# Optimization experiments

Measured on AMD Instinct MI355X. Metric: run time of the kernel, lower is better.

## Reference

```python
import jax, jax.numpy as jnp
import numpy as np

N = 50000
E = 400000
IN_DIM = 256
H1, D1 = 4, 128   # gat1: heads=4, hidden=128, concat -> 512
H2, D2 = 1, 64    # gat2: heads=1, out=64, concat=False
NEG_SLOPE = 0.2


def setup_inputs() -> dict:
    key = jax.random.key(0)
    ks = jax.random.split(key, 12)
    x = jax.random.normal(ks[0], (N, IN_DIM), dtype=jnp.float32)
    edge_index = jax.random.randint(ks[1], (2, E), 0, N, dtype=jnp.int64)
    edge_attr = jax.random.normal(ks[2], (E,), dtype=jnp.float32)
    # Glorot-ish init for weights, zeros for biases (as in PyG GATConv)
    def glorot(k, shape):
        fan = shape[0] + shape[-1]
        return jax.random.normal(k, shape, dtype=jnp.float32) * jnp.sqrt(2.0 / fan)
    W1 = glorot(ks[3], (IN_DIM, H1 * D1))
    a1_src = glorot(ks[4], (H1, D1))
    a1_dst = glorot(ks[5], (H1, D1))
    b1 = jnp.zeros((H1 * D1,), dtype=jnp.float32)
    W2 = glorot(ks[6], (H1 * D1, H2 * D2))
    a2_src = glorot(ks[7], (H2, D2))
    a2_dst = glorot(ks[8], (H2, D2))
    b2 = jnp.zeros((D2,), dtype=jnp.float32)
    return {"x": x, "edge_index": edge_index, "edge_attr": edge_attr,
            "W1": W1, "a1_src": a1_src, "a1_dst": a1_dst, "b1": b1,
            "W2": W2, "a2_src": a2_src, "a2_dst": a2_dst, "b2": b2}


def _gat_layer(x, src, dst, W, a_s, a_d, b, heads, d, concat):
    n = x.shape[0]
    h = (x @ W).reshape(n, heads, d)                      # [N,H,D]
    alpha_s = jnp.einsum('nhd,hd->nh', h, a_s)            # [N,H]
    alpha_d = jnp.einsum('nhd,hd->nh', h, a_d)
    e = jax.nn.leaky_relu(alpha_s[src] + alpha_d[dst], NEG_SLOPE)  # [Etot,H]
    # segment softmax over incoming edges of each dst node
    emax = jax.ops.segment_max(e, dst, num_segments=n)
    ex = jnp.exp(e - emax[dst])
    denom = jax.ops.segment_sum(ex, dst, num_segments=n)
    alpha = ex / (denom[dst] + 1e-16)                     # [Etot,H]
    msg = h[src] * alpha[:, :, None]                      # [Etot,H,D]
    out = jax.ops.segment_sum(msg, dst, num_segments=n)   # [N,H,D]
    out = out.reshape(n, heads * d) if concat else out.mean(axis=1)
    return out + b


def reference(x, edge_index, edge_attr, W1, a1_src, a1_dst, b1,
              W2, a2_src, a2_dst, b2):
    # edge_attr is ignored (GATConv built without edge_dim)
    loop = jnp.arange(N, dtype=edge_index.dtype)          # PyG add_self_loops=True
    src = jnp.concatenate([edge_index[0], loop])
    dst = jnp.concatenate([edge_index[1], loop])
    h = _gat_layer(x, src, dst, W1, a1_src, a1_dst, b1, H1, D1, True)
    h = jax.nn.elu(h)
    out = _gat_layer(h, src, dst, W2, a2_src, a2_dst, b2, H2, D2, False)
    return out
```

## Files before the change

### kernel.cpp

```cpp
#include <hip/hip_runtime.h>
#include <cstdint>

typedef unsigned short u16;
typedef short bf16x8_t __attribute__((ext_vector_type(8)));
typedef float f32x4_t __attribute__((ext_vector_type(4)));

#define DEVFN __device__ __forceinline__

DEVFN u16 f2bf(float f) {
  unsigned u = __builtin_bit_cast(unsigned, f);
  u = (u + 0x7fffu + ((u >> 16) & 1u)) >> 16;
  return (u16)u;
}
DEVFN float bf2f(u16 s) {
  unsigned u = ((unsigned)s) << 16;
  return __builtin_bit_cast(float, u);
}
DEVFN unsigned pk2bf(float a, float b) {
  return (unsigned)f2bf(a) | ((unsigned)f2bf(b) << 16);
}

DEVFN void gload_lds16(const u16* g, u16* l) {
  __builtin_amdgcn_global_load_lds(
      (const __attribute__((address_space(1))) void*)g,
      (__attribute__((address_space(3))) void*)l, 16, 0, 0);
}

__global__ void prep_kernel(const float* __restrict__ W1, const float* __restrict__ W2,
                            const int* __restrict__ edst,
                            u16* __restrict__ w1t, u16* __restrict__ w2t,
                            int* __restrict__ cnt, int e) {
  int b = blockIdx.x;
  if (b < 512) {
    int idx = b * 256 + threadIdx.x;
    int k = idx >> 9, m = idx & 511;
    w1t[m * 256 + k] = f2bf(W1[idx]);
  } else if (b < 512 + 128) {
    int idx = (b - 512) * 256 + threadIdx.x;
    int k = idx >> 6, m = idx & 63;
    w2t[m * 512 + k] = f2bf(W2[idx]);
  } else {
    int i = (b - 640) * 256 + threadIdx.x;
    if (i < e) atomicAdd(&cnt[edst[i]], 1);
  }
}

template<int BM, int BN, int WROWS, int K, int BK, int NP, int H, int DH>
__global__ __launch_bounds__(256) void gemm1_alpha_kernel(
    const float* __restrict__ A, const u16* __restrict__ BT, u16* __restrict__ C,
    const float* __restrict__ a_s, const float* __restrict__ a_d,
    float* __restrict__ as_out, float* __restrict__ ad_out, int M)
{
  constexpr int N = NP * BN;
  constexpr int WM = BM / WROWS;
  constexpr int MF = WM / 16;
  constexpr int NF = BN / 16;
  constexpr int KK = BK / 32;
  __shared__ __align__(16) u16 sA[BM][BK];
  __shared__ __align__(16) u16 sB[BN][BK];

  const int tid = threadIdx.x;
  const int lane = tid & 63;
  const int wr = tid >> 6;

  const int bid = blockIdx.x;
  const int xcd = bid & 7;
  const int rest = bid >> 3;
  const int p = rest & (NP - 1);
  const int rb = rest / NP;
  const int r = rb * 8 + xcd;
  const int NRB = (M + BM - 1) / BM;
  if (r >= NRB) return;
  const int brow = r * BM;
  const int bcol = p * BN;

  f32x4_t acc[MF][NF];
#pragma unroll
  for (int i = 0; i < MF; ++i)
#pragma unroll
    for (int j = 0; j < NF; ++j) acc[i][j] = f32x4_t{0.f, 0.f, 0.f, 0.f};

  const int rsel = lane & 15;
  const int kgrp = (lane >> 4) * 8;

#pragma unroll
  for (int k0 = 0; k0 < K; k0 += BK) {
    constexpr int RA = BM * BK / 2048;
#pragma unroll
    for (int c = 0; c < RA; ++c) {
      int q = c * 256 + tid;
      int row = q * 8 / BK;
      int col8 = (q * 8) % BK;
      int gr = brow + row; gr = gr < M ? gr : M - 1;
      const float* src = A + (size_t)gr * K + k0 + col8;
      float4 v0 = *reinterpret_cast<const float4*>(src);
      float4 v1 = *reinterpret_cast<const float4*>(src + 4);
      uint4 pk;
      pk.x = pk2bf(v0.x, v0.y);
      pk.y = pk2bf(v0.z, v0.w);
      pk.z = pk2bf(v1.x, v1.y);
      pk.w = pk2bf(v1.z, v1.w);
      *reinterpret_cast<uint4*>(&sA[row][col8]) = pk;
    }
    constexpr int RB = BN * BK / 2048;
#pragma unroll
    for (int c = 0; c < RB; ++c) {
      int t = c * 256 + tid;
      int row = t * 8 / BK;
      int col = (t * 8) % BK;
      gload_lds16(BT + (size_t)(bcol + row) * K + k0 + col, &sB[0][0] + t * 8);
    }
    __syncthreads();
#pragma unroll
    for (int kk = 0; kk < KK; ++kk) {
      bf16x8_t af[MF], bfr[NF];
#pragma unroll
      for (int i = 0; i < MF; ++i)
        af[i] = *reinterpret_cast<const bf16x8_t*>(&sA[wr * WM + i * 16 + rsel][kk * 32 + kgrp]);
#pragma unroll
      for (int j = 0; j < NF; ++j)
        bfr[j] = *reinterpret_cast<const bf16x8_t*>(&sB[j * 16 + rsel][kk * 32 + kgrp]);
#pragma unroll
      for (int i = 0; i < MF; ++i)
#pragma unroll
        for (int j = 0; j < NF; ++j)
          acc[i][j] = __builtin_amdgcn_mfma_f32_16x16x32_bf16(af[i], bfr[j], acc[i][j], 0, 0, 0);
    }
    __syncthreads();
  }

  const int crow0 = (lane >> 4) * 4;
  const int ccol = lane & 15;

#pragma unroll
  for (int i = 0; i < MF; ++i)
#pragma unroll
    for (int j = 0; j < NF; ++j)
#pragma unroll
      for (int rr = 0; rr < 4; ++rr) {
        int gr = brow + wr * WM + i * 16 + crow0 + rr;
        int gc = bcol + j * 16 + ccol;
        if (gr < M) C[(size_t)gr * N + gc] = f2bf(acc[i][j][rr]);
      }

  const int head = bcol / DH;
  float asv[NF], adv[NF];
#pragma unroll
  for (int j = 0; j < NF; ++j) {
    int gc = bcol + j * 16 + ccol;
    asv[j] = a_s[gc];
    adv[j] = a_d[gc];
  }
#pragma unroll
  for (int i = 0; i < MF; ++i) {
#pragma unroll
    for (int rr = 0; rr < 4; ++rr) {
      float ps = 0.f, pd = 0.f;
#pragma unroll
      for (int j = 0; j < NF; ++j) {
        float v = acc[i][j][rr];
        ps = fmaf(v, asv[j], ps);
        pd = fmaf(v, adv[j], pd);
      }
#pragma unroll
      for (int d = 1; d < 16; d <<= 1) {
        ps += __shfl_xor(ps, d, 64);
        pd += __shfl_xor(pd, d, 64);
      }
      if ((lane & 15) == 0) {
        int gr = brow + wr * WM + i * 16 + crow0 + rr;
        if (gr < M) {
          as_out[(size_t)gr * H + head] = ps;
          ad_out[(size_t)gr * H + head] = pd;
        }
      }
    }
  }
}

template<int BM, int BN, int WROWS, int K, int BK, int H, int DH>
__global__ __launch_bounds__(256) void gemm_alpha_kernel(
    const u16* __restrict__ A, const u16* __restrict__ BT, u16* __restrict__ C,
    const float* __restrict__ a_s, const float* __restrict__ a_d,
    float* __restrict__ as_out, float* __restrict__ ad_out, int M, int N)
{
  static_assert(BN == DH, "alpha store ownership");
  constexpr int WM = BM / WROWS;
  constexpr int MF = WM / 16;
  constexpr int NF = BN / 16;
  constexpr int KK = BK / 32;
  __shared__ __align__(16) u16 sA[BM][BK];
  __shared__ __align__(16) u16 sB[BN][BK];

  const int tid = threadIdx.x;
  const int lane = tid & 63;
  const int wr = tid >> 6;
  const int brow = blockIdx.x * BM;
  const int bcol = blockIdx.y * BN;

  f32x4_t acc[MF][NF];
#pragma unroll
  for (int i = 0; i < MF; ++i)
#pragma unroll
    for (int j = 0; j < NF; ++j) acc[i][j] = f32x4_t{0.f, 0.f, 0.f, 0.f};

  const int rsel = lane & 15;
  const int kgrp = (lane >> 4) * 8;

#pragma unroll
  for (int k0 = 0; k0 < K; k0 += BK) {
    constexpr int RA = BM * BK / 2048;
#pragma unroll
    for (int c = 0; c < RA; ++c) {
      int t = c * 256 + tid;
      int row = t * 8 / BK;
      int col = (t * 8) % BK;
      int gr = brow + row; gr = gr < M ? gr : M - 1;
      gload_lds16(A + (size_t)gr * K + k0 + col, &sA[0][0] + t * 8);
    }
    constexpr int RB = BN * BK / 2048;
#pragma unroll
    for (int c = 0; c < RB; ++c) {
      int t = c * 256 + tid;
      int row = t * 8 / BK;
      int col = (t * 8) % BK;
      gload_lds16(BT + (size_t)(bcol + row) * K + k0 + col, &sB[0][0] + t * 8);
    }
    __syncthreads();
#pragma unroll
    for (int kk = 0; kk < KK; ++kk) {
      bf16x8_t af[MF], bfr[NF];
#pragma unroll
      for (int i = 0; i < MF; ++i)
        af[i] = *reinterpret_cast<const bf16x8_t*>(&sA[wr * WM + i * 16 + rsel][kk * 32 + kgrp]);
#pragma unroll
      for (int j = 0; j < NF; ++j)
        bfr[j] = *reinterpret_cast<const bf16x8_t*>(&sB[j * 16 + rsel][kk * 32 + kgrp]);
#pragma unroll
      for (int i = 0; i < MF; ++i)
#pragma unroll
        for (int j = 0; j < NF; ++j)
          acc[i][j] = __builtin_amdgcn_mfma_f32_16x16x32_bf16(af[i], bfr[j], acc[i][j], 0, 0, 0);
    }
    __syncthreads();
  }

  const int crow0 = (lane >> 4) * 4;
  const int ccol = lane & 15;

#pragma unroll
  for (int i = 0; i < MF; ++i)
#pragma unroll
    for (int j = 0; j < NF; ++j)
#pragma unroll
      for (int rr = 0; rr < 4; ++rr) {
        int gr = brow + wr * WM + i * 16 + crow0 + rr;
        int gc = bcol + j * 16 + ccol;
        if (gr < M) C[(size_t)gr * N + gc] = f2bf(acc[i][j][rr]);
      }

  const int head = bcol / DH;
  float asv[NF], adv[NF];
#pragma unroll
  for (int j = 0; j < NF; ++j) {
    int gc = bcol + j * 16 + ccol;
    asv[j] = a_s[gc];
    adv[j] = a_d[gc];
  }
#pragma unroll
  for (int i = 0; i < MF; ++i) {
#pragma unroll
    for (int rr = 0; rr < 4; ++rr) {
      float ps = 0.f, pd = 0.f;
#pragma unroll
      for (int j = 0; j < NF; ++j) {
        float v = acc[i][j][rr];
        ps = fmaf(v, asv[j], ps);
        pd = fmaf(v, adv[j], pd);
      }
#pragma unroll
      for (int d = 1; d < 16; d <<= 1) {
        ps += __shfl_xor(ps, d, 64);
        pd += __shfl_xor(pd, d, 64);
      }
      if ((lane & 15) == 0) {
        int gr = brow + wr * WM + i * 16 + crow0 + rr;
        if (gr < M) {
          as_out[(size_t)gr * H + head] = ps;
          ad_out[(size_t)gr * H + head] = pd;
        }
      }
    }
  }
}

DEVFN int block_scan_256(int v, int tid, int* wsum) {
#pragma unroll
  for (int d = 1; d < 64; d <<= 1) {
    int u = __shfl_up(v, d, 64);
    if ((tid & 63) >= d) v += u;
  }
  if ((tid & 63) == 63) wsum[tid >> 6] = v;
  __syncthreads();
  int add = 0;
#pragma unroll
  for (int w = 0; w < 4; ++w) add += (w < (tid >> 6)) ? wsum[w] : 0;
  __syncthreads();
  return v + add;
}

__global__ __launch_bounds__(256) void scan_a_kernel(const int* __restrict__ cnt, int* __restrict__ bsum, int n) {
  __shared__ int ws4[4];
  int i = blockIdx.x * 256 + threadIdx.x;
  int v = (i < n) ? cnt[i] + 1 : 0;
  int incl = block_scan_256(v, threadIdx.x, ws4);
  if (threadIdx.x == 255) bsum[blockIdx.x] = incl;
}

__global__ __launch_bounds__(256) void scan_c_kernel(
    const int* __restrict__ cnt, const int* __restrict__ bsum,
    int* __restrict__ rowoff, int* __restrict__ cursor, int n)
{
  __shared__ int ws4[4];
  __shared__ int ws4b[4];
  __shared__ int base_sh;
  int pre = 0;
  for (int w = threadIdx.x; w < blockIdx.x; w += 256) pre += bsum[w];
#pragma unroll
  for (int d = 1; d < 64; d <<= 1) pre += __shfl_xor(pre, d, 64);
  if ((threadIdx.x & 63) == 0) ws4b[threadIdx.x >> 6] = pre;
  __syncthreads();
  if (threadIdx.x == 0) base_sh = ws4b[0] + ws4b[1] + ws4b[2] + ws4b[3];
  int i = blockIdx.x * 256 + threadIdx.x;
  int v = (i < n) ? cnt[i] + 1 : 0;
  int incl = block_scan_256(v, threadIdx.x, ws4);
  int off = base_sh + incl - v;
  if (i < n) {
    rowoff[i] = off;
    cursor[i] = off;
    if (i == n - 1) rowoff[n] = off + v;
  }
}

__global__ void scatter_kernel(const int* __restrict__ srcs, const int* __restrict__ dsts,
                               int* __restrict__ cursor, int* __restrict__ csr, int e, int n) {
  int i = blockIdx.x * 256 + threadIdx.x;
  if (i >= e + n) return;
  int s, d;
  if (i < e) { s = srcs[i]; d = dsts[i]; }
  else       { s = i - e; d = s; }
  int pos = atomicAdd(&cursor[d], 1);
  csr[pos] = s;
}

__global__ __launch_bounds__(256) void agg1_kernel(
    const u16* __restrict__ h1, const float* __restrict__ as1,
    const float* __restrict__ ad1, const int* __restrict__ rowoff,
    const int* __restrict__ csr, const float* __restrict__ b1,
    u16* __restrict__ out, int n)
{
  int node = (blockIdx.x * 256 + threadIdx.x) >> 6;
  int lane = threadIdx.x & 63;
  if (node >= n) return;
  const unsigned head = lane >> 4;
  const unsigned dimbase = lane * 8;
  int e0 = rowoff[node], e1 = rowoff[node + 1];
  float advn = ad1[((unsigned)node << 2) + head];

  float acc[8];
#pragma unroll
  for (int j = 0; j < 8; ++j) acc[j] = 0.f;
  float den = 0.f;

  for (int e = e0; e < e1; ++e) {
    unsigned s = (unsigned)csr[e];
    float t = as1[(s << 2) + head] + advn;
    float l = fmaxf(t, 0.2f * t);
    float ex = __expf(l);
    den += ex;
    bf16x8_t hv = *reinterpret_cast<const bf16x8_t*>(h1 + ((s << 9) + dimbase));
#pragma unroll
    for (int j = 0; j < 8; ++j) acc[j] = fmaf(ex, bf2f((u16)hv[j]), acc[j]);
  }

  float inv = 1.f / (den + 1e-16f);
  u16* orow = out + (((unsigned)node << 9) + dimbase);
#pragma unroll
  for (int j = 0; j < 8; ++j) {
    float v = acc[j] * inv + b1[dimbase + j];
    v = v > 0.f ? v : expm1f(v);
    orow[j] = f2bf(v);
  }
}

__global__ __launch_bounds__(256) void agg2_kernel(
    const u16* __restrict__ h2, const float* __restrict__ as2,
    const float* __restrict__ ad2, const int* __restrict__ rowoff,
    const int* __restrict__ csr, const float* __restrict__ b2,
    float* __restrict__ out, int n)
{
  int node = (blockIdx.x * 256 + threadIdx.x) >> 5;
  int l32 = threadIdx.x & 31;
  if (node >= n) return;
  int e0 = rowoff[node], e1 = rowoff[node + 1];
  float advn = ad2[node];

  float acc0 = 0.f, acc1 = 0.f, den = 0.f;
  for (int e = e0; e < e1; ++e) {
    unsigned s = (unsigned)csr[e];
    float t = as2[s] + advn;
    float l = fmaxf(t, 0.2f * t);
    float ex = __expf(l);
    den += ex;
    unsigned hv = *reinterpret_cast<const unsigned*>(h2 + (s << 6) + l32 * 2);
    acc0 = fmaf(ex, bf2f((u16)(hv & 0xffffu)), acc0);
    acc1 = fmaf(ex, bf2f((u16)(hv >> 16)), acc1);
  }
  float inv = 1.f / (den + 1e-16f);
  float2 o;
  o.x = acc0 * inv + b2[l32 * 2];
  o.y = acc1 * inv + b2[l32 * 2 + 1];
  *reinterpret_cast<float2*>(out + (((size_t)node) << 6) + l32 * 2) = o;
}

extern "C" void kernel_launch(void* const* d_in, const int* in_sizes, int n_in,
                              void* d_out, int out_size, void* d_ws, size_t ws_size,
                              hipStream_t stream) {
  const float* x   = (const float*)d_in[0];
  const int*   ei  = (const int*)d_in[1];
  const float* W1  = (const float*)d_in[3];
  const float* a1s = (const float*)d_in[4];
  const float* a1d = (const float*)d_in[5];
  const float* b1  = (const float*)d_in[6];
  const float* W2  = (const float*)d_in[7];
  const float* a2s = (const float*)d_in[8];
  const float* a2d = (const float*)d_in[9];
  const float* b2  = (const float*)d_in[10];
  float* out = (float*)d_out;

  const int IN_DIM = 256, H1D1 = 512, D2 = 64;
  const int N = in_sizes[0] / IN_DIM;
  const int E = in_sizes[1] / 2;

  char* ws = (char*)d_ws;
  size_t off = 0;
  auto alloc = [&](size_t bytes) -> void* {
    void* p = ws + off;
    off += (bytes + 255) & ~(size_t)255;
    return p;
  };
  u16*  w1t    = (u16*)alloc((size_t)H1D1 * IN_DIM * 2);
  u16*  w2t    = (u16*)alloc((size_t)D2 * H1D1 * 2);
  u16*  h1b    = (u16*)alloc((size_t)N * H1D1 * 2);
  int*  cnt    = (int*)alloc((size_t)N * 4);
  float* as1   = (float*)alloc((size_t)N * 4 * 4);
  float* ad1   = (float*)alloc((size_t)N * 4 * 4);
  float* as2   = (float*)alloc((size_t)N * 4);
  float* ad2   = (float*)alloc((size_t)N * 4);
  int*  cursor = (int*)alloc((size_t)N * 4);
  int*  rowoff = (int*)alloc((size_t)(N + 1) * 4);
  int*  bsum   = (int*)alloc(256 * 4);
  int*  csr    = (int*)alloc((size_t)(E + N) * 4);
  u16*  h1o    = (u16*)alloc((size_t)N * H1D1 * 2);
  u16*  h2b    = (u16*)alloc((size_t)N * D2 * 2);
  (void)n_in; (void)out_size; (void)ws_size;

  const int* esrc = ei;
  const int* edst = ei + E;

  (void)hipMemsetAsync(cnt, 0, (size_t)N * 4, stream);

  int eb = (E + 255) / 256;
  prep_kernel<<<640 + eb, 256, 0, stream>>>(W1, W2, edst, w1t, w2t, cnt, E);

  const int NRB = (N + 127) / 128;
  const int g1 = ((NRB + 7) / 8) * 8 * 4;
  gemm1_alpha_kernel<128, 128, 4, 256, 64, 4, 4, 128><<<g1, 256, 0, stream>>>(
      x, w1t, h1b, a1s, a1d, as1, ad1, N);

  int nsb = (N + 255) / 256;
  scan_a_kernel<<<nsb, 256, 0, stream>>>(cnt, bsum, N);
  scan_c_kernel<<<nsb, 256, 0, stream>>>(cnt, bsum, rowoff, cursor, N);
  scatter_kernel<<<(E + N + 255) / 256, 256, 0, stream>>>(esrc, edst, cursor, csr, E, N);

  agg1_kernel<<<(N + 3) / 4, 256, 0, stream>>>(h1b, as1, ad1, rowoff, csr, b1, h1o, N);

  dim3 g2((N + 63) / 64, 1);
  gemm_alpha_kernel<64, 64, 4, 512, 64, 1, 64><<<g2, 256, 0, stream>>>(
      h1o, w2t, h2b, a2s, a2d, as2, ad2, N, D2);

  agg2_kernel<<<((size_t)N * 32 + 255) / 256, 256, 0, stream>>>(h2b, as2, ad2, rowoff, csr, b2, out, N);
}
```

Baseline: 245.7 us.

## Reorder layer-1 as aggregate-then-project using precomputed attention weight vectors

```diff
diff --git a/kernel.cpp b/kernel.cpp
--- a/kernel.cpp
+++ b/kernel.cpp
@@ -27,31 +27,186 @@
 }
 
 __global__ void prep_kernel(const float* __restrict__ W1, const float* __restrict__ W2,
+                            const float* __restrict__ a1s, const float* __restrict__ a1d,
                             const int* __restrict__ edst,
                             u16* __restrict__ w1t, u16* __restrict__ w2t,
+                            float* __restrict__ ws1, float* __restrict__ wd1,
                             int* __restrict__ cnt, int e) {
   int b = blockIdx.x;
   if (b < 512) {
     int idx = b * 256 + threadIdx.x;
     int k = idx >> 9, m = idx & 511;
     w1t[m * 256 + k] = f2bf(W1[idx]);
-  } else if (b < 512 + 128) {
+  } else if (b < 640) {
     int idx = (b - 512) * 256 + threadIdx.x;
     int k = idx >> 6, m = idx & 63;
     w2t[m * 512 + k] = f2bf(W2[idx]);
+  } else if (b < 648) {
+    int b2 = b - 640;
+    int h = b2 >> 1;
+    int isD = b2 & 1;
+    const float* av = (isD ? a1d : a1s) + h * 128;
+    int k = threadIdx.x;
+    float sum = 0.f;
+#pragma unroll 8
+    for (int d = 0; d < 128; ++d)
+      sum = fmaf(W1[k * 512 + h * 128 + d], av[d], sum);
+    (isD ? wd1 : ws1)[h * 256 + k] = sum;
   } else {
-    int i = (b - 640) * 256 + threadIdx.x;
+    int i = (b - 648) * 256 + threadIdx.x;
     if (i < e) atomicAdd(&cnt[edst[i]], 1);
   }
 }
 
-template<int BM, int BN, int WROWS, int K, int BK, int NP, int H, int DH>
-__global__ __launch_bounds__(256) void gemm1_alpha_kernel(
-    const float* __restrict__ A, const u16* __restrict__ BT, u16* __restrict__ C,
-    const float* __restrict__ a_s, const float* __restrict__ a_d,
-    float* __restrict__ as_out, float* __restrict__ ad_out, int M)
+__global__ __launch_bounds__(256) void conv_alpha_kernel(
+    const float* __restrict__ x, const float* __restrict__ ws1, const float* __restrict__ wd1,
+    u16* __restrict__ xb, float* __restrict__ as1, float* __restrict__ ad1, int n)
 {
-  constexpr int N = NP * BN;
+  int node = (blockIdx.x * 256 + threadIdx.x) >> 6;
+  int lane = threadIdx.x & 63;
+  if (node >= n) return;
+  float4 xv = *reinterpret_cast<const float4*>(x + (size_t)node * 256 + lane * 4);
+  uint2 pk;
+  pk.x = pk2bf(xv.x, xv.y);
+  pk.y = pk2bf(xv.z, xv.w);
+  *reinterpret_cast<uint2*>(xb + (size_t)node * 256 + lane * 4) = pk;
+
+  float p[8];
+#pragma unroll
+  for (int v = 0; v < 8; ++v) {
+    const float* wv = (v < 4 ? ws1 : wd1) + (v & 3) * 256 + lane * 4;
+    float4 w4 = *reinterpret_cast<const float4*>(wv);
+    p[v] = xv.x * w4.x + xv.y * w4.y + xv.z * w4.z + xv.w * w4.w;
+  }
+#pragma unroll
+  for (int d = 1; d < 64; d <<= 1) {
+#pragma unroll
+    for (int v = 0; v < 8; ++v) p[v] += __shfl_xor(p[v], d, 64);
+  }
+  if (lane == 0) {
+    *reinterpret_cast<float4*>(as1 + (size_t)node * 4) = make_float4(p[0], p[1], p[2], p[3]);
+    *reinterpret_cast<float4*>(ad1 + (size_t)node * 4) = make_float4(p[4], p[5], p[6], p[7]);
+  }
+}
+
+DEVFN int block_scan_256(int v, int tid, int* wsum) {
+#pragma unroll
+  for (int d = 1; d < 64; d <<= 1) {
+    int u = __shfl_up(v, d, 64);
+    if ((tid & 63) >= d) v += u;
+  }
+  if ((tid & 63) == 63) wsum[tid >> 6] = v;
+  __syncthreads();
+  int add = 0;
+#pragma unroll
+  for (int w = 0; w < 4; ++w) add += (w < (tid >> 6)) ? wsum[w] : 0;
+  __syncthreads();
+  return v + add;
+}
+
+__global__ __launch_bounds__(256) void scan_a_kernel(const int* __restrict__ cnt, int* __restrict__ bsum, int n) {
+  __shared__ int ws4[4];
+  int i = blockIdx.x * 256 + threadIdx.x;
+  int v = (i < n) ? cnt[i] + 1 : 0;
+  int incl = block_scan_256(v, threadIdx.x, ws4);
+  if (threadIdx.x == 255) bsum[blockIdx.x] = incl;
+}
+
+__global__ __launch_bounds__(256) void scan_c_kernel(
+    const int* __restrict__ cnt, const int* __restrict__ bsum,
+    int* __restrict__ rowoff, int* __restrict__ cursor, int n)
+{
+  __shared__ int ws4[4];
+  __shared__ int ws4b[4];
+  __shared__ int base_sh;
+  int pre = 0;
+  for (int w = threadIdx.x; w < blockIdx.x; w += 256) pre += bsum[w];
+#pragma unroll
+  for (int d = 1; d < 64; d <<= 1) pre += __shfl_xor(pre, d, 64);
+  if ((threadIdx.x & 63) == 0) ws4b[threadIdx.x >> 6] = pre;
+  __syncthreads();
+  if (threadIdx.x == 0) base_sh = ws4b[0] + ws4b[1] + ws4b[2] + ws4b[3];
+  int i = blockIdx.x * 256 + threadIdx.x;
+  int v = (i < n) ? cnt[i] + 1 : 0;
+  int incl = block_scan_256(v, threadIdx.x, ws4);
+  int off = base_sh + incl - v;
+  if (i < n) {
+    rowoff[i] = off;
+    cursor[i] = off;
+    if (i == n - 1) rowoff[n] = off + v;
+  }
+}
+
+__global__ void scatter_kernel(const int* __restrict__ srcs, const int* __restrict__ dsts,
+                               int* __restrict__ cursor, int* __restrict__ csr, int e, int n) {
+  int i = blockIdx.x * 256 + threadIdx.x;
+  if (i >= e + n) return;
+  int s, d;
+  if (i < e) { s = srcs[i]; d = dsts[i]; }
+  else       { s = i - e; d = s; }
+  int pos = atomicAdd(&cursor[d], 1);
+  csr[pos] = s;
+}
+
+__global__ __launch_bounds__(256) void aggx_kernel(
+    const u16* __restrict__ xb, const float* __restrict__ as1,
+    const float* __restrict__ ad1, const int* __restrict__ rowoff,
+    const int* __restrict__ csr, u16* __restrict__ aggx, size_t plane, int n)
+{
+  int node = (blockIdx.x * 256 + threadIdx.x) >> 6;
+  int lane = threadIdx.x & 63;
+  if (node >= n) return;
+  int e0 = rowoff[node], e1 = rowoff[node + 1];
+  float4 adv = *reinterpret_cast<const float4*>(ad1 + (size_t)node * 4);
+  const unsigned dimb = (unsigned)lane * 4;
+
+  float acc[4][4];
+#pragma unroll
+  for (int h = 0; h < 4; ++h)
+#pragma unroll
+    for (int d = 0; d < 4; ++d) acc[h][d] = 0.f;
+  float den[4] = {0.f, 0.f, 0.f, 0.f};
+
+  for (int e = e0; e < e1; ++e) {
+    unsigned s = (unsigned)csr[e];
+    float4 a4 = *reinterpret_cast<const float4*>(as1 + ((size_t)s << 2));
+    float ex[4];
+    {
+      float t0 = a4.x + adv.x, t1 = a4.y + adv.y, t2 = a4.z + adv.z, t3 = a4.w + adv.w;
+      ex[0] = __expf(fmaxf(t0, 0.2f * t0));
+      ex[1] = __expf(fmaxf(t1, 0.2f * t1));
+      ex[2] = __expf(fmaxf(t2, 0.2f * t2));
+      ex[3] = __expf(fmaxf(t3, 0.2f * t3));
+    }
+#pragma unroll
+    for (int h = 0; h < 4; ++h) den[h] += ex[h];
+    uint2 xv = *reinterpret_cast<const uint2*>(xb + (((size_t)s << 8) + dimb));
+    float xf[4];
+    xf[0] = bf2f((u16)(xv.x & 0xffffu));
+    xf[1] = bf2f((u16)(xv.x >> 16));
+    xf[2] = bf2f((u16)(xv.y & 0xffffu));
+    xf[3] = bf2f((u16)(xv.y >> 16));
+#pragma unroll
+    for (int h = 0; h < 4; ++h)
+#pragma unroll
+      for (int d = 0; d < 4; ++d) acc[h][d] = fmaf(ex[h], xf[d], acc[h][d]);
+  }
+
+#pragma unroll
+  for (int h = 0; h < 4; ++h) {
+    float inv = 1.f / (den[h] + 1e-16f);
+    uint2 o;
+    o.x = pk2bf(acc[h][0] * inv, acc[h][1] * inv);
+    o.y = pk2bf(acc[h][2] * inv, acc[h][3] * inv);
+    *reinterpret_cast<uint2*>(aggx + (size_t)h * plane + ((size_t)node << 8) + dimb) = o;
+  }
+}
+
+template<int BM, int BN, int WROWS, int K, int BK>
+__global__ __launch_bounds__(256) void gemm1_kernel(
+    const u16* __restrict__ Aall, const u16* __restrict__ BT,
+    const float* __restrict__ b1, u16* __restrict__ C, int M, size_t plane)
+{
   constexpr int WM = BM / WROWS;
   constexpr int MF = WM / 16;
   constexpr int NF = BN / 16;
@@ -62,17 +217,9 @@
   const int tid = threadIdx.x;
   const int lane = tid & 63;
   const int wr = tid >> 6;
-
-  const int bid = blockIdx.x;
-  const int xcd = bid & 7;
-  const int rest = bid >> 3;
-  const int p = rest & (NP - 1);
-  const int rb = rest / NP;
-  const int r = rb * 8 + xcd;
-  const int NRB = (M + BM - 1) / BM;
-  if (r >= NRB) return;
-  const int brow = r * BM;
-  const int bcol = p * BN;
+  const int brow = blockIdx.x * BM;
+  const int bcol = blockIdx.y * BN;
+  const u16* A = Aall + blockIdx.y * plane;
 
   f32x4_t acc[MF][NF];
 #pragma unroll
@@ -88,19 +235,11 @@
     constexpr int RA = BM * BK / 2048;
 #pragma unroll
     for (int c = 0; c < RA; ++c) {
-      int q = c * 256 + tid;
-      int row = q * 8 / BK;
-      int col8 = (q * 8) % BK;
+      int t = c * 256 + tid;
+      int row = t * 8 / BK;
+      int col = (t * 8) % BK;
       int gr = brow + row; gr = gr < M ? gr : M - 1;
-      const float* src = A + (size_t)gr * K + k0 + col8;
-      float4 v0 = *reinterpret_cast<const float4*>(src);
-      float4 v1 = *reinterpret_cast<const float4*>(src + 4);
-      uint4 pk;
-      pk.x = pk2bf(v0.x, v0.y);
-      pk.y = pk2bf(v0.z, v0.w);
-      pk.z = pk2bf(v1.x, v1.y);
-      pk.w = pk2bf(v1.z, v1.w);
-      *reinterpret_cast<uint4*>(&sA[row][col8]) = pk;
+      gload_lds16(A + (size_t)gr * K + k0 + col, &sA[0][0] + t * 8);
     }
     constexpr int RB = BN * BK / 2048;
 #pragma unroll
@@ -131,7 +270,6 @@
 
   const int crow0 = (lane >> 4) * 4;
   const int ccol = lane & 15;
-
 #pragma unroll
   for (int i = 0; i < MF; ++i)
 #pragma unroll
@@ -140,42 +278,12 @@
       for (int rr = 0; rr < 4; ++rr) {
         int gr = brow + wr * WM + i * 16 + crow0 + rr;
         int gc = bcol + j * 16 + ccol;
-        if (gr < M) C[(size_t)gr * N + gc] = f2bf(acc[i][j][rr]);
-      }
-
-  const int head = bcol / DH;
-  float asv[NF], adv[NF];
-#pragma unroll
-  for (int j = 0; j < NF; ++j) {
-    int gc = bcol + j * 16 + ccol;
-    asv[j] = a_s[gc];
-    adv[j] = a_d[gc];
-  }
-#pragma unroll
-  for (int i = 0; i < MF; ++i) {
-#pragma unroll
-    for (int rr = 0; rr < 4; ++rr) {
-      float ps = 0.f, pd = 0.f;
-#pragma unroll
-      for (int j = 0; j < NF; ++j) {
-        float v = acc[i][j][rr];
-        ps = fmaf(v, asv[j], ps);
-        pd = fmaf(v, adv[j], pd);
-      }
-#pragma unroll
-      for (int d = 1; d < 16; d <<= 1) {
-        ps += __shfl_xor(ps, d, 64);
-        pd += __shfl_xor(pd, d, 64);
-      }
-      if ((lane & 15) == 0) {
-        int gr = brow + wr * WM + i * 16 + crow0 + rr;
         if (gr < M) {
-          as_out[(size_t)gr * H + head] = ps;
-          ad_out[(size_t)gr * H + head] = pd;
+          float v = acc[i][j][rr] + b1[gc];
+          v = v > 0.f ? v : expm1f(v);
+          C[(size_t)gr * 512 + gc] = f2bf(v);
         }
       }
-    }
-  }
 }
 
 template<int BM, int BN, int WROWS, int K, int BK, int H, int DH>
@@ -291,105 +399,6 @@
         }
       }
     }
-  }
-}
-
-DEVFN int block_scan_256(int v, int tid, int* wsum) {
-#pragma unroll
-  for (int d = 1; d < 64; d <<= 1) {
-    int u = __shfl_up(v, d, 64);
-    if ((tid & 63) >= d) v += u;
-  }
-  if ((tid & 63) == 63) wsum[tid >> 6] = v;
-  __syncthreads();
-  int add = 0;
-#pragma unroll
-  for (int w = 0; w < 4; ++w) add += (w < (tid >> 6)) ? wsum[w] : 0;
-  __syncthreads();
-  return v + add;
-}
-
-__global__ __launch_bounds__(256) void scan_a_kernel(const int* __restrict__ cnt, int* __restrict__ bsum, int n) {
-  __shared__ int ws4[4];
-  int i = blockIdx.x * 256 + threadIdx.x;
-  int v = (i < n) ? cnt[i] + 1 : 0;
-  int incl = block_scan_256(v, threadIdx.x, ws4);
-  if (threadIdx.x == 255) bsum[blockIdx.x] = incl;
-}
-
-__global__ __launch_bounds__(256) void scan_c_kernel(
-    const int* __restrict__ cnt, const int* __restrict__ bsum,
-    int* __restrict__ rowoff, int* __restrict__ cursor, int n)
-{
-  __shared__ int ws4[4];
-  __shared__ int ws4b[4];
-  __shared__ int base_sh;
-  int pre = 0;
-  for (int w = threadIdx.x; w < blockIdx.x; w += 256) pre += bsum[w];
-#pragma unroll
-  for (int d = 1; d < 64; d <<= 1) pre += __shfl_xor(pre, d, 64);
-  if ((threadIdx.x & 63) == 0) ws4b[threadIdx.x >> 6] = pre;
-  __syncthreads();
-  if (threadIdx.x == 0) base_sh = ws4b[0] + ws4b[1] + ws4b[2] + ws4b[3];
-  int i = blockIdx.x * 256 + threadIdx.x;
-  int v = (i < n) ? cnt[i] + 1 : 0;
-  int incl = block_scan_256(v, threadIdx.x, ws4);
-  int off = base_sh + incl - v;
-  if (i < n) {
-    rowoff[i] = off;
-    cursor[i] = off;
-    if (i == n - 1) rowoff[n] = off + v;
-  }
-}
-
-__global__ void scatter_kernel(const int* __restrict__ srcs, const int* __restrict__ dsts,
-                               int* __restrict__ cursor, int* __restrict__ csr, int e, int n) {
-  int i = blockIdx.x * 256 + threadIdx.x;
-  if (i >= e + n) return;
-  int s, d;
-  if (i < e) { s = srcs[i]; d = dsts[i]; }
-  else       { s = i - e; d = s; }
-  int pos = atomicAdd(&cursor[d], 1);
-  csr[pos] = s;
-}
-
-__global__ __launch_bounds__(256) void agg1_kernel(
-    const u16* __restrict__ h1, const float* __restrict__ as1,
-    const float* __restrict__ ad1, const int* __restrict__ rowoff,
-    const int* __restrict__ csr, const float* __restrict__ b1,
-    u16* __restrict__ out, int n)
-{
-  int node = (blockIdx.x * 256 + threadIdx.x) >> 6;
-  int lane = threadIdx.x & 63;
-  if (node >= n) return;
-  const unsigned head = lane >> 4;
-  const unsigned dimbase = lane * 8;
-  int e0 = rowoff[node], e1 = rowoff[node + 1];
-  float advn = ad1[((unsigned)node << 2) + head];
-
-  float acc[8];
-#pragma unroll
-  for (int j = 0; j < 8; ++j) acc[j] = 0.f;
-  float den = 0.f;
-
-  for (int e = e0; e < e1; ++e) {
-    unsigned s = (unsigned)csr[e];
-    float t = as1[(s << 2) + head] + advn;
-    float l = fmaxf(t, 0.2f * t);
-    float ex = __expf(l);
-    den += ex;
-    bf16x8_t hv = *reinterpret_cast<const bf16x8_t*>(h1 + ((s << 9) + dimbase));
-#pragma unroll
-    for (int j = 0; j < 8; ++j) acc[j] = fmaf(ex, bf2f((u16)hv[j]), acc[j]);
-  }
-
-  float inv = 1.f / (den + 1e-16f);
-  u16* orow = out + (((unsigned)node << 9) + dimbase);
-#pragma unroll
-  for (int j = 0; j < 8; ++j) {
-    float v = acc[j] * inv + b1[dimbase + j];
-    v = v > 0.f ? v : expm1f(v);
-    orow[j] = f2bf(v);
   }
 }
 
@@ -451,19 +460,24 @@
   };
   u16*  w1t    = (u16*)alloc((size_t)H1D1 * IN_DIM * 2);
   u16*  w2t    = (u16*)alloc((size_t)D2 * H1D1 * 2);
-  u16*  h1b    = (u16*)alloc((size_t)N * H1D1 * 2);
-  int*  cnt    = (int*)alloc((size_t)N * 4);
+  float* ws1   = (float*)alloc(4 * 256 * 4);
+  float* wd1   = (float*)alloc(4 * 256 * 4);
+  u16*  xb     = (u16*)alloc((size_t)N * IN_DIM * 2);
   float* as1   = (float*)alloc((size_t)N * 4 * 4);
   float* ad1   = (float*)alloc((size_t)N * 4 * 4);
-  float* as2   = (float*)alloc((size_t)N * 4);
-  float* ad2   = (float*)alloc((size_t)N * 4);
+  int*  cnt    = (int*)alloc((size_t)N * 4);
   int*  cursor = (int*)alloc((size_t)N * 4);
   int*  rowoff = (int*)alloc((size_t)(N + 1) * 4);
   int*  bsum   = (int*)alloc(256 * 4);
   int*  csr    = (int*)alloc((size_t)(E + N) * 4);
+  size_t plane = (size_t)N * IN_DIM;
+  u16*  aggx   = (u16*)alloc(4 * plane * 2);
   u16*  h1o    = (u16*)alloc((size_t)N * H1D1 * 2);
-  u16*  h2b    = (u16*)alloc((size_t)N * D2 * 2);
   (void)n_in; (void)out_size; (void)ws_size;
+
+  u16*   h2b = xb;
+  float* as2 = (float*)(xb + (size_t)N * D2);
+  float* ad2 = as2 + N;
 
   const int* esrc = ei;
   const int* edst = ei + E;
@@ -471,19 +485,19 @@
   (void)hipMemsetAsync(cnt, 0, (size_t)N * 4, stream);
 
   int eb = (E + 255) / 256;
-  prep_kernel<<<640 + eb, 256, 0, stream>>>(W1, W2, edst, w1t, w2t, cnt, E);
-
-  const int NRB = (N + 127) / 128;
-  const int g1 = ((NRB + 7) / 8) * 8 * 4;
-  gemm1_alpha_kernel<128, 128, 4, 256, 64, 4, 4, 128><<<g1, 256, 0, stream>>>(
-      x, w1t, h1b, a1s, a1d, as1, ad1, N);
+  prep_kernel<<<648 + eb, 256, 0, stream>>>(W1, W2, a1s, a1d, edst, w1t, w2t, ws1, wd1, cnt, E);
+
+  conv_alpha_kernel<<<(N + 3) / 4, 256, 0, stream>>>(x, ws1, wd1, xb, as1, ad1, N);
 
   int nsb = (N + 255) / 256;
   scan_a_kernel<<<nsb, 256, 0, stream>>>(cnt, bsum, N);
   scan_c_kernel<<<nsb, 256, 0, stream>>>(cnt, bsum, rowoff, cursor, N);
   scatter_kernel<<<(E + N + 255) / 256, 256, 0, stream>>>(esrc, edst, cursor, csr, E, N);
 
-  agg1_kernel<<<(N + 3) / 4, 256, 0, stream>>>(h1b, as1, ad1, rowoff, csr, b1, h1o, N);
+  aggx_kernel<<<(N + 3) / 4, 256, 0, stream>>>(xb, as1, ad1, rowoff, csr, aggx, plane, N);
+
+  dim3 g1((N + 127) / 128, 4);
+  gemm1_kernel<128, 128, 4, 256, 64><<<g1, 256, 0, stream>>>(aggx, w1t, b1, h1o, N, plane);
 
   dim3 g2((N + 63) / 64, 1);
   gemm_alpha_kernel<64, 64, 4, 512, 64, 1, 64><<<g2, 256, 0, stream>>>(
```

Result: slower. 269.2 us (+9.5%).
